# Kernel tuning notes

Measured on AMD Instinct MI355X. Metric: run time of the kernel, lower is better.

## Reference

```python
import jax, jax.numpy as jnp
import numpy as np

B, S, N, H, F, L, Lt = 2, 8, 150, 128, 40, 2, 1
EF = 2 * F + 2  # 82: src feat + dst feat + distance + bond
_rows_np, _cols_np = np.where(~np.eye(N, dtype=bool))  # fully connected, no self loops
_rows = jnp.asarray(_rows_np)
_cols = jnp.asarray(_cols_np)
E = _rows_np.shape[0]


def setup_inputs() -> dict:
    key = jax.random.key(0)
    ks = jax.random.split(key, 20)
    w = lambda k, shape: 0.1 * jax.random.normal(k, shape, dtype=jnp.float32)
    d = {}
    d['t'] = jax.random.uniform(ks[0], (B, 1), dtype=jnp.float32)
    d['x'] = jax.random.normal(ks[1], (B, S, N, 3), dtype=jnp.float32)
    d['peptide_seq'] = jax.random.randint(ks[2], (B, 15), 0, 20)
    d['atom_labels'] = jax.random.randint(ks[3], (B, N), 0, 5)
    d['amino_acid_pos'] = jax.random.randint(ks[4], (B, N), 1, 16)
    d['bond_matrix'] = (jax.random.uniform(ks[5], (B, N, N)) < 0.1).astype(jnp.float32)
    d['edge_mask'] = jnp.ones((B, N, N), jnp.float32)
    d['atom_mask'] = jnp.ones((B, N, 1), jnp.float32)
    d['restore_indices'] = jnp.tile(jnp.eye(N, dtype=jnp.float32)[None], (B, 1, 1))
    d['W_e1'] = w(ks[6], (L, EF, H)); d['b_e1'] = jnp.zeros((L, H), jnp.float32)
    d['W_e2'] = w(ks[7], (L, H, H)); d['b_e2'] = jnp.zeros((L, H), jnp.float32)
    d['W_c'] = w(ks[8], (L, H, 1)); d['b_c'] = jnp.zeros((L, 1), jnp.float32)
    d['W_h'] = w(ks[9], (L, F + H, F)); d['b_h'] = jnp.zeros((L, F), jnp.float32)
    d['w_t'] = w(ks[10], (L, 1, H)); d['w_b_t'] = jnp.zeros((L, H), jnp.float32)
    d['tW_e1'] = w(ks[11], (Lt, EF, H)); d['tb_e1'] = jnp.zeros((Lt, H), jnp.float32)
    d['tW_e2'] = w(ks[12], (Lt, H, H)); d['tb_e2'] = jnp.zeros((Lt, H), jnp.float32)
    d['tW_c'] = w(ks[13], (Lt, H, 1)); d['tb_c'] = jnp.zeros((Lt, 1), jnp.float32)
    d['tW_h'] = w(ks[14], (Lt, F + H, F)); d['tb_h'] = jnp.zeros((Lt, F), jnp.float32)
    return d


def _forward(t, x, peptide_seq, atom_labels, amino_acid_pos, bond_matrix, edge_mask,
             atom_mask, restore_indices, W_e1, b_e1, W_e2, b_e2, W_c, b_c, W_h, b_h,
             w_t, w_b_t, tW_e1, tb_e1, tW_e2, tb_e2, tW_c, tb_c, tW_h, tb_h):
    # single-atom embedding: [B, N, 40]
    aa = jnp.take_along_axis(peptide_seq, amino_acid_pos - 1, axis=1)
    emb = jnp.concatenate([
        jax.nn.one_hot(atom_labels, 5, dtype=x.dtype),
        jax.nn.one_hot(aa, 20, dtype=x.dtype),
        jax.nn.one_hot(amino_acid_pos - 1, 15, dtype=x.dtype)], axis=-1)
    h = jnp.broadcast_to(emb[:, None], (B, S, N, F))
    # restore absolute coordinates: x[b,s,i,d] = sum_j x[b,s,j,d] * R[b,i,j]
    x = jnp.einsum('bsjd,bij->bsid', x, restore_indices)
    x0 = x
    # per-edge masks/features (gathered once; identical math to full cdist + indexing)
    em_e = edge_mask.reshape(B, 1, N * N)[:, :, _rows * N + _cols][..., None]  # [B,1,E,1]
    bond_e = jnp.broadcast_to(bond_matrix[:, _rows, _cols][:, None, :, None], (B, S, E, 1))

    def layer(x, h, We1, be1, We2, be2, Wc, bc, Wh, bh, temb):
        diff = x[:, :, _rows] - x[:, :, _cols]                      # [B,S,E,3]
        dist = jnp.sqrt(jnp.sum(diff * diff, -1, keepdims=True) + 1e-12)
        ef = jnp.concatenate([h[:, :, _rows], h[:, :, _cols], dist, bond_e], -1)  # [B,S,E,82]
        m = jax.nn.silu(ef @ We1 + be1 + temb)
        m = jax.nn.silu(m @ We2 + be2) * em_e                        # [B,S,E,H]
        cw = m @ Wc + bc                                             # [B,S,E,1]
        x_out = jnp.zeros_like(x).at[:, :, _rows].add(diff * cw) / (N - 1)
        agg = jnp.zeros((B, S, N, m.shape[-1]), m.dtype).at[:, :, _rows].add(m)
        h_out = jax.nn.silu(jnp.concatenate([h, agg], -1) @ Wh + bh)
        return x_out, h_out

    for l in range(L):
        temb = (t @ w_t[l] + w_b_t[l])[:, None, None, :]             # [B,1,1,H]
        xo, h = layer(x, h, W_e1[l], b_e1[l], W_e2[l], b_e2[l], W_c[l], b_c[l], W_h[l], b_h[l], temb)
        x = x + xo
    for l in range(Lt):
        xo, h = layer(x, h, tW_e1[l], tb_e1[l], tW_e2[l], tb_e2[l], tW_c[l], tb_c[l], tW_h[l], tb_h[l], 0.0)
        x = x + xo
    return (x - x0) * atom_mask[:, None, :, :]


def reference(t, x, peptide_seq, atom_labels, amino_acid_pos, bond_matrix, edge_mask,
              atom_mask, restore_indices, W_e1, b_e1, W_e2, b_e2, W_c, b_c, W_h, b_h,
              w_t, w_b_t, tW_e1, tb_e1, tW_e2, tb_e2, tW_c, tb_c, tW_h, tb_h):
    return _forward(t, x, peptide_seq, atom_labels, amino_acid_pos, bond_matrix, edge_mask,
                    atom_mask, restore_indices, W_e1, b_e1, W_e2, b_e2, W_c, b_c, W_h, b_h,
                    w_t, w_b_t, tW_e1, tb_e1, tW_e2, tb_e2, tW_c, tb_c, tW_h, tb_h)
```

## Files before the change

kernel.cpp:

```cpp
#include <hip/hip_runtime.h>
#include <math.h>

#define B_ 2
#define S_ 8
#define N_ 150
#define H_ 128
#define F_ 40
#define EF_ 82
#define NP_ 160
#define MPQ 136

typedef __attribute__((ext_vector_type(8))) short short8;
typedef __attribute__((ext_vector_type(4))) float float4v;

__device__ __forceinline__ float silu_f(float v) {
    return v * __builtin_amdgcn_rcpf(1.0f + __expf(-v));
}

__device__ __forceinline__ unsigned short f2bf(float f) {
    unsigned u = __builtin_bit_cast(unsigned, f);
    return (unsigned short)((u + 0x7fffu + ((u >> 16) & 1u)) >> 16);
}

__global__ void prelude_kernel(const float* __restrict__ w0,
                               const float* __restrict__ w1,
                               const float* __restrict__ w2,
                               unsigned short* __restrict__ we2t,
                               const float* __restrict__ x,
                               const float* __restrict__ R,
                               float* __restrict__ xa,
                               float* __restrict__ x0,
                               const int* __restrict__ pep,
                               const int* __restrict__ labels,
                               const int* __restrict__ aapos,
                               const float* __restrict__ We1,
                               const float* __restrict__ be1,
                               const float* __restrict__ tp,
                               const float* __restrict__ wt,
                               const float* __restrict__ wbt,
                               float* __restrict__ h0,
                               float* __restrict__ Af,
                               float* __restrict__ Bf) {
    int bid = blockIdx.x;
    int tid = threadIdx.x;
    if (bid < 192) {
        int e = bid * 256 + tid;
        int l = e >> 14, idx = e & 16383;
        int k = idx >> 7, c = idx & 127;
        const float* src = (l == 0) ? w0 : (l == 1) ? w1 : w2;
        we2t[l * 16384 + c * H_ + k] = f2bf(src[idx]);
    } else if (bid < 221) {
        int idx = (bid - 192) * 256 + tid;
        if (idx < B_ * S_ * N_ * 3) {
            int d = idx % 3;
            int i = (idx / 3) % N_;
            int bs = idx / (3 * N_);
            int b = bs / S_;
            const float* xrow = x + bs * N_ * 3 + d;
            const float* Rrow = R + (b * N_ + i) * N_;
            float acc = 0.0f;
            for (int j = 0; j < N_; j++) acc += xrow[j * 3] * Rrow[j];
            xa[idx] = acc;
            x0[idx] = acc;
        }
    } else {
        int rel = bid - 221;
        int bi = rel * 2 + (tid >> 7);
        int b = bi / N_, i = bi % N_;
        int c = tid & 127;
        int al = labels[bi];
        int ap = aapos[bi];
        int aa = pep[b * 15 + ap - 1];
        int r0 = al, r1 = 5 + aa, r2 = 25 + ap - 1;
        float fa = We1[r0 * H_ + c] + We1[r1 * H_ + c] + We1[r2 * H_ + c]
                 + be1[c] + tp[b] * wt[c] + wbt[c];
        float fb = We1[(F_ + r0) * H_ + c] + We1[(F_ + r1) * H_ + c] + We1[(F_ + r2) * H_ + c];
        float hv = 0.0f;
        if (c < F_) hv = (c == r0 || c == r1 || c == r2) ? 1.0f : 0.0f;
        for (int s = 0; s < S_; s++) {
            int n = (b * S_ + s) * N_ + i;
            Af[n * H_ + c] = fa;
            Bf[n * H_ + c] = fb;
            if (c < F_) h0[n * F_ + c] = hv;
        }
    }
}

__global__ __launch_bounds__(256, 4) void edge_fused_kernel(
    const float* __restrict__ x_in,
    const float* __restrict__ Afeat,
    const float* __restrict__ Bfeat,
    const float* __restrict__ We1,
    const unsigned short* __restrict__ we2t,
    const float* __restrict__ be2,
    const float* __restrict__ Wc,
    const float* __restrict__ bcp,
    const float* __restrict__ bond,
    const float* __restrict__ emask,
    const float* __restrict__ h_in,
    const float* __restrict__ Wh,
    const float* __restrict__ bh,
    const float* __restrict__ We1n,
    const float* __restrict__ be1n,
    const float* __restrict__ tp,
    const float* __restrict__ wtn,
    const float* __restrict__ wbtn,
    int has_t,
    const float* __restrict__ x0v,
    const float* __restrict__ amask,
    int final_mode,
    float* __restrict__ x_out,
    float* __restrict__ h_out,
    float* __restrict__ Af_out,
    float* __restrict__ Bf_out)
{
    __shared__ __align__(16) short mbuf[2][16 * MPQ];
    __shared__ float4 diffE[NP_];
    __shared__ float2 dbL[NP_];
    __shared__ float DsumL[3];
    __shared__ float wpart[4][3];
    __shared__ float catL[F_ + H_];
    __shared__ float partL[120];
    __shared__ float hnewL[F_];

    int blk = blockIdx.x;
    int i = blk % N_, bs = blk / N_, b = bs / S_;
    int tid = threadIdx.x;
    int node = bs * N_ + i;
    int lane = tid & 63, w = tid >> 6;
    int qd = lane >> 4, l15 = lane & 15;
    int rowLoc = tid >> 4, c0 = (tid & 15) * 8;

    float xi0 = x_in[node * 3 + 0];
    float xi1 = x_in[node * 3 + 1];
    float xi2 = x_in[node * 3 + 2];

    if (tid < NP_) {
        int j = tid;
        float xj0 = xi0, xj1 = xi1, xj2 = xi2, bnd = 0.0f, emv = 0.0f;
        if (j < N_) {
            int nj = bs * N_ + j;
            xj0 = x_in[nj * 3 + 0];
            xj1 = x_in[nj * 3 + 1];
            xj2 = x_in[nj * 3 + 2];
            int eij = (b * N_ + i) * N_ + j;
            bnd = bond[eij];
            emv = (j == i) ? 0.0f : emask[eij];
        }
        float d0 = xi0 - xj0, d1 = xi1 - xj1, d2 = xi2 - xj2;
        diffE[j] = make_float4(d0, d1, d2, emv);
        dbL[j] = make_float2(sqrtf(d0 * d0 + d1 * d1 + d2 * d2 + 1e-12f), bnd);
    }

    float afr[8], w80r[8], w81r[8];
    {
        float4 t0 = *(const float4*)&Afeat[node * H_ + c0];
        float4 t1 = *(const float4*)&Afeat[node * H_ + c0 + 4];
        afr[0]=t0.x; afr[1]=t0.y; afr[2]=t0.z; afr[3]=t0.w;
        afr[4]=t1.x; afr[5]=t1.y; afr[6]=t1.z; afr[7]=t1.w;
        t0 = *(const float4*)&We1[80 * H_ + c0];
        t1 = *(const float4*)&We1[80 * H_ + c0 + 4];
        w80r[0]=t0.x; w80r[1]=t0.y; w80r[2]=t0.z; w80r[3]=t0.w;
        w80r[4]=t1.x; w80r[5]=t1.y; w80r[6]=t1.z; w80r[7]=t1.w;
        t0 = *(const float4*)&We1[81 * H_ + c0];
        t1 = *(const float4*)&We1[81 * H_ + c0 + 4];
        w81r[0]=t0.x; w81r[1]=t0.y; w81r[2]=t0.z; w81r[3]=t0.w;
        w81r[4]=t1.x; w81r[5]=t1.y; w81r[6]=t1.z; w81r[7]=t1.w;
    }

    int ctb = w * 2;
    float b2r0 = be2[ctb * 16 + l15],  b2r1 = be2[ctb * 16 + 16 + l15];
    float wc0  = Wc[ctb * 16 + l15],   wc1  = Wc[ctb * 16 + 16 + l15];
    const unsigned short* bb0 = we2t + (ctb * 16 + l15) * H_ + qd * 8;
    const unsigned short* bb1 = bb0 + 16 * H_;
    short8 bf00 = *(const short8*)(bb0 +  0);
    short8 bf01 = *(const short8*)(bb0 + 32);
    short8 bf02 = *(const short8*)(bb0 + 64);
    short8 bf03 = *(const short8*)(bb0 + 96);
    short8 bf10 = *(const short8*)(bb1 +  0);
    short8 bf11 = *(const short8*)(bb1 + 32);
    short8 bf12 = *(const short8*)(bb1 + 64);
    short8 bf13 = *(const short8*)(bb1 + 96);

    __syncthreads();

    if (w == 0) {
        float p0 = 0, p1 = 0, p2 = 0;
        for (int j = lane; j < NP_; j += 64) {
            float4 d = diffE[j];
            p0 += d.x; p1 += d.y; p2 += d.z;
        }
        for (int s = 1; s < 64; s <<= 1) {
            p0 += __shfl_xor(p0, s, 64);
            p1 += __shfl_xor(p1, s, 64);
            p2 += __shfl_xor(p2, s, 64);
        }
        if (lane == 0) { DsumL[0] = p0; DsumL[1] = p1; DsumL[2] = p2; }
    }

    float aggP0 = 0, aggP1 = 0;
    float SP00 = 0, SP01 = 0, SP02 = 0, SP10 = 0, SP11 = 0, SP12 = 0;

    for (int jt = 0; jt < 10; jt++) {
        short* mb = mbuf[jt & 1];
        int jrow = jt * 16 + rowLoc;
        float mv[8];
        if (jrow < N_) {
            const float* bp = &Bfeat[(bs * N_ + jrow) * H_ + c0];
            float4 b0 = *(const float4*)bp;
            float4 b1 = *(const float4*)(bp + 4);
            float br[8] = {b0.x, b0.y, b0.z, b0.w, b1.x, b1.y, b1.z, b1.w};
            float2 db = dbL[jrow];
#pragma unroll
            for (int u = 0; u < 8; u++)
                mv[u] = silu_f(afr[u] + br[u] + db.x * w80r[u] + db.y * w81r[u]);
        } else {
#pragma unroll
            for (int u = 0; u < 8; u++) mv[u] = 0.0f;
        }
        short8 pkv;
#pragma unroll
        for (int u = 0; u < 8; u++) pkv[u] = (short)f2bf(mv[u]);
        *(short8*)&mb[rowLoc * MPQ + c0] = pkv;
        __syncthreads();

        const short* arow = &mb[l15 * MPQ + qd * 8];
        short8 a0 = *(const short8*)(arow +  0);
        short8 a1 = *(const short8*)(arow + 32);
        short8 a2 = *(const short8*)(arow + 64);
        short8 a3 = *(const short8*)(arow + 96);
        float4v acc0 = {0, 0, 0, 0}, acc1 = {0, 0, 0, 0};
        acc0 = __builtin_amdgcn_mfma_f32_16x16x32_bf16(a0, bf00, acc0, 0, 0, 0);
        acc1 = __builtin_amdgcn_mfma_f32_16x16x32_bf16(a0, bf10, acc1, 0, 0, 0);
        acc0 = __builtin_amdgcn_mfma_f32_16x16x32_bf16(a1, bf01, acc0, 0, 0, 0);
        acc1 = __builtin_amdgcn_mfma_f32_16x16x32_bf16(a1, bf11, acc1, 0, 0, 0);
        acc0 = __builtin_amdgcn_mfma_f32_16x16x32_bf16(a2, bf02, acc0, 0, 0, 0);
        acc1 = __builtin_amdgcn_mfma_f32_16x16x32_bf16(a2, bf12, acc1, 0, 0, 0);
        acc0 = __builtin_amdgcn_mfma_f32_16x16x32_bf16(a3, bf03, acc0, 0, 0, 0);
        acc1 = __builtin_amdgcn_mfma_f32_16x16x32_bf16(a3, bf13, acc1, 0, 0, 0);

#pragma unroll
        for (int r = 0; r < 4; r++) {
            int j = jt * 16 + qd * 4 + r;
            float4 de = diffE[j];
            float mv0 = silu_f(acc0[r] + b2r0) * de.w;
            float mv1 = silu_f(acc1[r] + b2r1) * de.w;
            aggP0 += mv0; aggP1 += mv1;
            SP00 += de.x * mv0; SP01 += de.y * mv0; SP02 += de.z * mv0;
            SP10 += de.x * mv1; SP11 += de.y * mv1; SP12 += de.z * mv1;
        }
    }

#define QR_(v) { v += __shfl_xor(v, 16, 64); v += __shfl_xor(v, 32, 64); }
    QR_(aggP0) QR_(aggP1)
    QR_(SP00) QR_(SP01) QR_(SP02)
    QR_(SP10) QR_(SP11) QR_(SP12)
#undef QR_

    if (!final_mode) {
        if (qd == 0) {
            catL[F_ + ctb * 16 + l15]      = aggP0;
            catL[F_ + ctb * 16 + 16 + l15] = aggP1;
        }
        if (tid < F_) catL[tid] = h_in[node * F_ + tid];
    }

    float p0 = wc0 * SP00 + wc1 * SP10;
    float p1 = wc0 * SP01 + wc1 * SP11;
    float p2 = wc0 * SP02 + wc1 * SP12;
    for (int s = 1; s < 16; s <<= 1) {
        p0 += __shfl_xor(p0, s, 64);
        p1 += __shfl_xor(p1, s, 64);
        p2 += __shfl_xor(p2, s, 64);
    }
    if (lane == 0) { wpart[w][0] = p0; wpart[w][1] = p1; wpart[w][2] = p2; }
    __syncthreads();
    if (tid < 3) {
        float tot = wpart[0][tid] + wpart[1][tid] + wpart[2][tid] + wpart[3][tid]
                  + bcp[0] * DsumL[tid];
        float xn = x_in[node * 3 + tid] + tot * (1.0f / (float)(N_ - 1));
        if (final_mode)
            x_out[node * 3 + tid] = (xn - x0v[node * 3 + tid]) * amask[b * N_ + i];
        else
            x_out[node * 3 + tid] = xn;
    }

    if (final_mode) return;

    if (tid < 120) {
        int f = tid % 40, ks = tid / 40;
        float p = 0.0f;
        int k0 = ks * 56;
#pragma unroll 8
        for (int k = k0; k < k0 + 56; k++) p += catL[k] * Wh[k * F_ + f];
        partL[tid] = p;
    }
    __syncthreads();
    if (tid < F_) {
        float hv = silu_f(partL[tid] + partL[40 + tid] + partL[80 + tid] + bh[tid]);
        hnewL[tid] = hv;
        h_out[node * F_ + tid] = hv;
    }
    __syncthreads();
    if (tid < H_) {
        float fa = be1n[tid] + (has_t ? tp[b] * wtn[tid] + wbtn[tid] : 0.0f);
        float fb = 0.0f;
#pragma unroll 8
        for (int k = 0; k < F_; k++) {
            float hv = hnewL[k];
            fa += hv * We1n[k * H_ + tid];
            fb += hv * We1n[(F_ + k) * H_ + tid];
        }
        Af_out[node * H_ + tid] = fa;
        Bf_out[node * H_ + tid] = fb;
    }
}

extern "C" void kernel_launch(void* const* d_in, const int* in_sizes, int n_in,
                              void* d_out, int out_size, void* d_ws, size_t ws_size,
                              hipStream_t stream) {
    const float* t     = (const float*)d_in[0];
    const float* x     = (const float*)d_in[1];
    const int*   pep   = (const int*)d_in[2];
    const int*   labels= (const int*)d_in[3];
    const int*   aapos = (const int*)d_in[4];
    const float* bond  = (const float*)d_in[5];
    const float* em    = (const float*)d_in[6];
    const float* amask = (const float*)d_in[7];
    const float* R     = (const float*)d_in[8];
    const float* W_e1  = (const float*)d_in[9];
    const float* b_e1  = (const float*)d_in[10];
    const float* W_e2  = (const float*)d_in[11];
    const float* b_e2  = (const float*)d_in[12];
    const float* W_c   = (const float*)d_in[13];
    const float* b_c   = (const float*)d_in[14];
    const float* W_h   = (const float*)d_in[15];
    const float* b_h   = (const float*)d_in[16];
    const float* w_t   = (const float*)d_in[17];
    const float* w_b_t = (const float*)d_in[18];
    const float* tW_e1 = (const float*)d_in[19];
    const float* tb_e1 = (const float*)d_in[20];
    const float* tW_e2 = (const float*)d_in[21];
    const float* tb_e2 = (const float*)d_in[22];
    const float* tW_c  = (const float*)d_in[23];
    const float* tb_c  = (const float*)d_in[24];
    float* out = (float*)d_out;

    float* ws = (float*)d_ws;
    unsigned short* we2t = (unsigned short*)ws;
    float* x0  = ws + 24576;
    float* xA  = x0 + 7200;
    float* xB  = xA + 7200;
    float* hA  = xB + 7200;
    float* hB  = hA + 96000;
    float* Af1 = hB + 96000;
    float* Bf1 = Af1 + 307200;
    float* Af2 = Bf1 + 307200;
    float* Bf2 = Af2 + 307200;

    const int NB = B_ * S_ * N_;

    prelude_kernel<<<371, 256, 0, stream>>>(W_e2, W_e2 + H_ * H_, tW_e2, we2t,
                                            x, R, xA, x0,
                                            pep, labels, aapos, W_e1, b_e1,
                                            t, w_t, w_b_t, hA, Af1, Bf1);

    edge_fused_kernel<<<NB, 256, 0, stream>>>(
        xA, Af1, Bf1, W_e1, we2t, b_e2, W_c, b_c, bond, em,
        hA, W_h, b_h, W_e1 + EF_ * H_, b_e1 + H_, t, w_t + H_, w_b_t + H_, 1,
        nullptr, nullptr, 0,
        xB, hB, Af2, Bf2);

    edge_fused_kernel<<<NB, 256, 0, stream>>>(
        xB, Af2, Bf2, W_e1 + EF_ * H_, we2t + 16384, b_e2 + H_, W_c + H_, b_c + 1,
        bond, em,
        hB, W_h + (F_ + H_) * F_, b_h + F_, tW_e1, tb_e1, nullptr, nullptr, nullptr, 0,
        nullptr, nullptr, 0,
        xA, hA, Af1, Bf1);

    edge_fused_kernel<<<NB, 256, 0, stream>>>(
        xA, Af1, Bf1, tW_e1, we2t + 32768, tb_e2, tW_c, tb_c, bond, em,
        nullptr, nullptr, nullptr, nullptr, nullptr, nullptr, nullptr, nullptr, 0,
        x0, amask, 1,
        out, nullptr, nullptr, nullptr);
}
```

Before: 269.9 us.

## Process 32-row edge tiles with register prefetch and pre-transposed node weights

The edge loop now handles two 16-row message tiles per barrier, taking it from 10 to 5 iterations, and prefetches the next Bfeat rows into registers so global load latency overlaps the MFMA work. The prelude additionally transposes W_h and the next layer's W_e1 node rows so the per-node update can use float4 contiguous weight loads. The A/B feature projection is also split across all 256 threads instead of 128. This costs more LDS (doubled mbuf) and more registers, which may affect occupancy at 4 waves per EU.

```diff
diff --git a/kernel.cpp b/kernel.cpp
--- a/kernel.cpp
+++ b/kernel.cpp
@@ -9,6 +9,7 @@
 #define EF_ 82
 #define NP_ 160
 #define MPQ 136
+#define NB_ 2400
 
 typedef __attribute__((ext_vector_type(8))) short short8;
 typedef __attribute__((ext_vector_type(4))) float float4v;
@@ -22,9 +23,8 @@
     return (unsigned short)((u + 0x7fffu + ((u >> 16) & 1u)) >> 16);
 }
 
-__global__ void prelude_kernel(const float* __restrict__ w0,
-                               const float* __restrict__ w1,
-                               const float* __restrict__ w2,
+__global__ void prelude_kernel(const float* __restrict__ W_e2,
+                               const float* __restrict__ tW_e2,
                                unsigned short* __restrict__ we2t,
                                const float* __restrict__ x,
                                const float* __restrict__ R,
@@ -40,14 +40,19 @@
                                const float* __restrict__ wbt,
                                float* __restrict__ h0,
                                float* __restrict__ Af,
-                               float* __restrict__ Bf) {
+                               float* __restrict__ Bf,
+                               const float* __restrict__ W_h,
+                               float* __restrict__ whT,
+                               const float* __restrict__ We1L1,
+                               const float* __restrict__ tWe1,
+                               float* __restrict__ w1nT) {
     int bid = blockIdx.x;
     int tid = threadIdx.x;
     if (bid < 192) {
         int e = bid * 256 + tid;
         int l = e >> 14, idx = e & 16383;
         int k = idx >> 7, c = idx & 127;
-        const float* src = (l == 0) ? w0 : (l == 1) ? w1 : w2;
+        const float* src = (l == 0) ? W_e2 : (l == 1) ? (W_e2 + H_ * H_) : tW_e2;
         we2t[l * 16384 + c * H_ + k] = f2bf(src[idx]);
     } else if (bid < 221) {
         int idx = (bid - 192) * 256 + tid;
@@ -63,7 +68,7 @@
             xa[idx] = acc;
             x0[idx] = acc;
         }
-    } else {
+    } else if (bid < 371) {
         int rel = bid - 221;
         int bi = rel * 2 + (tid >> 7);
         int b = bi / N_, i = bi % N_;
@@ -83,24 +88,38 @@
             Bf[n * H_ + c] = fb;
             if (c < F_) h0[n * F_ + c] = hv;
         }
+    } else if (bid < 424) {
+        int e = (bid - 371) * 256 + tid;
+        if (e < 2 * F_ * 168) {
+            int l = e / 6720, idx = e % 6720;
+            int f = idx / 168, k = idx % 168;
+            whT[l * 6720 + f * 168 + k] = W_h[l * 6720 + k * F_ + f];
+        }
+    } else {
+        int e = (bid - 424) * 256 + tid;
+        int s = e / 10240, idx = e % 10240;
+        int c = idx / 80, k = idx % 80;
+        const float* src = s ? tWe1 : We1L1;
+        w1nT[s * 10240 + c * 80 + k] = src[k * H_ + c];
     }
 }
 
-__global__ __launch_bounds__(256, 4) void edge_fused_kernel(
+__global__ __attribute__((amdgpu_flat_work_group_size(256, 256), amdgpu_waves_per_eu(4, 4)))
+void edge_v4_kernel(
     const float* __restrict__ x_in,
     const float* __restrict__ Afeat,
     const float* __restrict__ Bfeat,
     const float* __restrict__ We1,
-    const unsigned short* __restrict__ we2t,
+    const unsigned short* __restrict__ we2p,
     const float* __restrict__ be2,
     const float* __restrict__ Wc,
     const float* __restrict__ bcp,
     const float* __restrict__ bond,
     const float* __restrict__ emask,
     const float* __restrict__ h_in,
-    const float* __restrict__ Wh,
+    const float* __restrict__ whTp,
     const float* __restrict__ bh,
-    const float* __restrict__ We1n,
+    const float* __restrict__ w1nTp,
     const float* __restrict__ be1n,
     const float* __restrict__ tp,
     const float* __restrict__ wtn,
@@ -114,7 +133,7 @@
     float* __restrict__ Af_out,
     float* __restrict__ Bf_out)
 {
-    __shared__ __align__(16) short mbuf[2][16 * MPQ];
+    __shared__ __align__(16) short mbuf[2][32 * MPQ];
     __shared__ float4 diffE[NP_];
     __shared__ float2 dbL[NP_];
     __shared__ float DsumL[3];
@@ -171,7 +190,7 @@
     int ctb = w * 2;
     float b2r0 = be2[ctb * 16 + l15],  b2r1 = be2[ctb * 16 + 16 + l15];
     float wc0  = Wc[ctb * 16 + l15],   wc1  = Wc[ctb * 16 + 16 + l15];
-    const unsigned short* bb0 = we2t + (ctb * 16 + l15) * H_ + qd * 8;
+    const unsigned short* bb0 = we2p + (ctb * 16 + l15) * H_ + qd * 8;
     const unsigned short* bb1 = bb0 + 16 * H_;
     short8 bf00 = *(const short8*)(bb0 +  0);
     short8 bf01 = *(const short8*)(bb0 + 32);
@@ -182,6 +201,16 @@
     short8 bf12 = *(const short8*)(bb1 + 64);
     short8 bf13 = *(const short8*)(bb1 + 96);
 
+    float4 p0a, p0b, p1a, p1b;
+    {
+        int jr0 = rowLoc;
+        const float* bp = &Bfeat[(bs * N_ + jr0) * H_ + c0];
+        p0a = *(const float4*)bp; p0b = *(const float4*)(bp + 4);
+        int jr1 = rowLoc + 16;
+        bp = &Bfeat[(bs * N_ + jr1) * H_ + c0];
+        p1a = *(const float4*)bp; p1b = *(const float4*)(bp + 4);
+    }
+
     __syncthreads();
 
     if (w == 0) {
@@ -201,30 +230,8 @@
     float aggP0 = 0, aggP1 = 0;
     float SP00 = 0, SP01 = 0, SP02 = 0, SP10 = 0, SP11 = 0, SP12 = 0;
 
-    for (int jt = 0; jt < 10; jt++) {
-        short* mb = mbuf[jt & 1];
-        int jrow = jt * 16 + rowLoc;
-        float mv[8];
-        if (jrow < N_) {
-            const float* bp = &Bfeat[(bs * N_ + jrow) * H_ + c0];
-            float4 b0 = *(const float4*)bp;
-            float4 b1 = *(const float4*)(bp + 4);
-            float br[8] = {b0.x, b0.y, b0.z, b0.w, b1.x, b1.y, b1.z, b1.w};
-            float2 db = dbL[jrow];
-#pragma unroll
-            for (int u = 0; u < 8; u++)
-                mv[u] = silu_f(afr[u] + br[u] + db.x * w80r[u] + db.y * w81r[u]);
-        } else {
-#pragma unroll
-            for (int u = 0; u < 8; u++) mv[u] = 0.0f;
-        }
-        short8 pkv;
-#pragma unroll
-        for (int u = 0; u < 8; u++) pkv[u] = (short)f2bf(mv[u]);
-        *(short8*)&mb[rowLoc * MPQ + c0] = pkv;
-        __syncthreads();
-
-        const short* arow = &mb[l15 * MPQ + qd * 8];
+    auto do_tile = [&](short* mb, int t16, int stb) {
+        const short* arow = &mb[(t16 + l15) * MPQ + qd * 8];
         short8 a0 = *(const short8*)(arow +  0);
         short8 a1 = *(const short8*)(arow + 32);
         short8 a2 = *(const short8*)(arow + 64);
@@ -238,17 +245,66 @@
         acc1 = __builtin_amdgcn_mfma_f32_16x16x32_bf16(a2, bf12, acc1, 0, 0, 0);
         acc0 = __builtin_amdgcn_mfma_f32_16x16x32_bf16(a3, bf03, acc0, 0, 0, 0);
         acc1 = __builtin_amdgcn_mfma_f32_16x16x32_bf16(a3, bf13, acc1, 0, 0, 0);
-
 #pragma unroll
         for (int r = 0; r < 4; r++) {
-            int j = jt * 16 + qd * 4 + r;
+            int j = stb + t16 + qd * 4 + r;
             float4 de = diffE[j];
-            float mv0 = silu_f(acc0[r] + b2r0) * de.w;
-            float mv1 = silu_f(acc1[r] + b2r1) * de.w;
-            aggP0 += mv0; aggP1 += mv1;
-            SP00 += de.x * mv0; SP01 += de.y * mv0; SP02 += de.z * mv0;
-            SP10 += de.x * mv1; SP11 += de.y * mv1; SP12 += de.z * mv1;
-        }
+            float m0 = silu_f(acc0[r] + b2r0) * de.w;
+            float m1 = silu_f(acc1[r] + b2r1) * de.w;
+            aggP0 += m0; aggP1 += m1;
+            SP00 += de.x * m0; SP01 += de.y * m0; SP02 += de.z * m0;
+            SP10 += de.x * m1; SP11 += de.y * m1; SP12 += de.z * m1;
+        }
+    };
+
+    for (int st = 0; st < 5; st++) {
+        int stb = st * 32;
+        short* mb = mbuf[st & 1];
+        int jrow0 = stb + rowLoc;
+        int jrow1 = jrow0 + 16;
+        float mv0[8], mv1[8];
+        if (jrow0 < N_) {
+            float br[8] = {p0a.x, p0a.y, p0a.z, p0a.w, p0b.x, p0b.y, p0b.z, p0b.w};
+            float2 db = dbL[jrow0];
+#pragma unroll
+            for (int u = 0; u < 8; u++)
+                mv0[u] = silu_f(afr[u] + br[u] + db.x * w80r[u] + db.y * w81r[u]);
+        } else {
+#pragma unroll
+            for (int u = 0; u < 8; u++) mv0[u] = 0.0f;
+        }
+        if (jrow1 < N_) {
+            float br[8] = {p1a.x, p1a.y, p1a.z, p1a.w, p1b.x, p1b.y, p1b.z, p1b.w};
+            float2 db = dbL[jrow1];
+#pragma unroll
+            for (int u = 0; u < 8; u++)
+                mv1[u] = silu_f(afr[u] + br[u] + db.x * w80r[u] + db.y * w81r[u]);
+        } else {
+#pragma unroll
+            for (int u = 0; u < 8; u++) mv1[u] = 0.0f;
+        }
+        short8 pk0, pk1;
+#pragma unroll
+        for (int u = 0; u < 8; u++) { pk0[u] = (short)f2bf(mv0[u]); pk1[u] = (short)f2bf(mv1[u]); }
+        *(short8*)&mb[rowLoc * MPQ + c0] = pk0;
+        *(short8*)&mb[(rowLoc + 16) * MPQ + c0] = pk1;
+        __syncthreads();
+
+        if (st < 4) {
+            int nr0 = stb + 32 + rowLoc;
+            const float* bp = &Bfeat[(bs * N_ + nr0) * H_ + c0];
+            p0a = *(const float4*)bp; p0b = *(const float4*)(bp + 4);
+            int nr1 = stb + 48 + rowLoc;
+            if (nr1 < N_) {
+                bp = &Bfeat[(bs * N_ + nr1) * H_ + c0];
+                p1a = *(const float4*)bp; p1b = *(const float4*)(bp + 4);
+            } else {
+                p1a = make_float4(0.f, 0.f, 0.f, 0.f); p1b = p1a;
+            }
+        }
+
+        do_tile(mb, 0, stb);
+        do_tile(mb, 16, stb);
     }
 
 #define QR_(v) { v += __shfl_xor(v, 16, 64); v += __shfl_xor(v, 32, 64); }
@@ -289,10 +345,17 @@
 
     if (tid < 120) {
         int f = tid % 40, ks = tid / 40;
+        int k0 = ks * 56;
+        const float* wr = whTp + f * 168 + k0;
         float p = 0.0f;
-        int k0 = ks * 56;
-#pragma unroll 8
-        for (int k = k0; k < k0 + 56; k++) p += catL[k] * Wh[k * F_ + f];
+#pragma unroll
+        for (int k = 0; k < 56; k += 4) {
+            float4 wv = *(const float4*)(wr + k);
+            p += catL[k0 + k]     * wv.x;
+            p += catL[k0 + k + 1] * wv.y;
+            p += catL[k0 + k + 2] * wv.z;
+            p += catL[k0 + k + 3] * wv.w;
+        }
         partL[tid] = p;
     }
     __syncthreads();
@@ -302,17 +365,22 @@
         h_out[node * F_ + tid] = hv;
     }
     __syncthreads();
-    if (tid < H_) {
-        float fa = be1n[tid] + (has_t ? tp[b] * wtn[tid] + wbtn[tid] : 0.0f);
-        float fb = 0.0f;
-#pragma unroll 8
-        for (int k = 0; k < F_; k++) {
-            float hv = hnewL[k];
-            fa += hv * We1n[k * H_ + tid];
-            fb += hv * We1n[(F_ + k) * H_ + tid];
-        }
-        Af_out[node * H_ + tid] = fa;
-        Bf_out[node * H_ + tid] = fb;
+    {
+        int c = tid & 127;
+        int isB = tid >> 7;
+        float acc = isB ? 0.0f
+                        : (be1n[c] + (has_t ? tp[b] * wtn[c] + wbtn[c] : 0.0f));
+        const float* wr = w1nTp + c * 80 + isB * 40;
+#pragma unroll
+        for (int k = 0; k < 40; k += 4) {
+            float4 wv = *(const float4*)(wr + k);
+            acc += hnewL[k]     * wv.x;
+            acc += hnewL[k + 1] * wv.y;
+            acc += hnewL[k + 2] * wv.z;
+            acc += hnewL[k + 3] * wv.w;
+        }
+        float* dst = isB ? Bf_out : Af_out;
+        dst[node * H_ + c] = acc;
     }
 }
 
@@ -348,37 +416,38 @@
 
     float* ws = (float*)d_ws;
     unsigned short* we2t = (unsigned short*)ws;
-    float* x0  = ws + 24576;
-    float* xA  = x0 + 7200;
-    float* xB  = xA + 7200;
-    float* hA  = xB + 7200;
-    float* hB  = hA + 96000;
-    float* Af1 = hB + 96000;
-    float* Bf1 = Af1 + 307200;
-    float* Af2 = Bf1 + 307200;
-    float* Bf2 = Af2 + 307200;
-
-    const int NB = B_ * S_ * N_;
-
-    prelude_kernel<<<371, 256, 0, stream>>>(W_e2, W_e2 + H_ * H_, tW_e2, we2t,
-                                            x, R, xA, x0,
+    float* x0   = ws + 24576;
+    float* xA   = x0 + 7200;
+    float* xB   = xA + 7200;
+    float* hA   = xB + 7200;
+    float* hB   = hA + 96000;
+    float* Af1  = hB + 96000;
+    float* Bf1  = Af1 + 307200;
+    float* Af2  = Bf1 + 307200;
+    float* Bf2  = Af2 + 307200;
+    float* whT  = Bf2 + 307200;
+    float* w1nT = whT + 13440;
+
+    prelude_kernel<<<504, 256, 0, stream>>>(W_e2, tW_e2, we2t, x, R, xA, x0,
                                             pep, labels, aapos, W_e1, b_e1,
-                                            t, w_t, w_b_t, hA, Af1, Bf1);
-
-    edge_fused_kernel<<<NB, 256, 0, stream>>>(
+                                            t, w_t, w_b_t, hA, Af1, Bf1,
+                                            W_h, whT,
+                                            W_e1 + EF_ * H_, tW_e1, w1nT);
+
+    edge_v4_kernel<<<NB_, 256, 0, stream>>>(
         xA, Af1, Bf1, W_e1, we2t, b_e2, W_c, b_c, bond, em,
-        hA, W_h, b_h, W_e1 + EF_ * H_, b_e1 + H_, t, w_t + H_, w_b_t + H_, 1,
+        hA, whT, b_h, w1nT, b_e1 + H_, t, w_t + H_, w_b_t + H_, 1,
         nullptr, nullptr, 0,
         xB, hB, Af2, Bf2);
 
-    edge_fused_kernel<<<NB, 256, 0, stream>>>(
+    edge_v4_kernel<<<NB_, 256, 0, stream>>>(
         xB, Af2, Bf2, W_e1 + EF_ * H_, we2t + 16384, b_e2 + H_, W_c + H_, b_c + 1,
         bond, em,
-        hB, W_h + (F_ + H_) * F_, b_h + F_, tW_e1, tb_e1, nullptr, nullptr, nullptr, 0,
+        hB, whT + 6720, b_h + F_, w1nT + 10240, tb_e1, nullptr, nullptr, nullptr, 0,
         nullptr, nullptr, 0,
         xA, hA, Af1, Bf1);
 
-    edge_fused_kernel<<<NB, 256, 0, stream>>>(
+    edge_v4_kernel<<<NB_, 256, 0, stream>>>(
         xA, Af1, Bf1, tW_e1, we2t + 32768, tb_e2, tW_c, tb_c, bond, em,
         nullptr, nullptr, nullptr, nullptr, nullptr, nullptr, nullptr, nullptr, 0,
         x0, amask, 1,
```

After: 859.7 us. 219% more time.
